# Kernel optimization log

Measured on AMD Instinct MI355X. Metric: run time of the kernel, lower is better.

## Reference

```python
import jax, jax.numpy as jnp
import numpy as np
from math import factorial

N_NODES = 20000
N_EDGES = 80000
NUM_GRAPHS = 64
NUM_NEIGHBORS = 3.8
POOL_NODES = 4.0  # num_nodes=4 constant in source forward

# ---------------- real Wigner 3j (e3nn-style, Frobenius norm 1) ----------------

def _w3j_complex(j1, j2, j3, m1, m2, m3):
    if m1 + m2 + m3 != 0:
        return 0.0
    t1 = j2 - m1 - j3; t2 = j1 + m2 - j3; t3 = j1 + j2 - j3
    t4 = j1 - m1; t5 = j2 + m2
    tmin = max(0, t1, t2); tmax = min(t3, t4, t5)
    if tmin > tmax:
        return 0.0
    s = 0.0
    for t in range(tmin, tmax + 1):
        s += (-1.0) ** t / (factorial(t) * factorial(t - t1) * factorial(t - t2)
                            * factorial(t3 - t) * factorial(t4 - t) * factorial(t5 - t))
    tri = (factorial(j1 + j2 - j3) * factorial(j1 - j2 + j3) * factorial(-j1 + j2 + j3)
           / factorial(j1 + j2 + j3 + 1))
    norm = np.sqrt(tri * factorial(j1 + m1) * factorial(j1 - m1) * factorial(j2 + m2)
                   * factorial(j2 - m2) * factorial(j3 + m3) * factorial(j3 - m3))
    return (-1.0) ** (j1 - j2 - m3) * norm * s


def _real_basis(l):
    U = np.zeros((2 * l + 1, 2 * l + 1), dtype=np.complex128)
    U[l, l] = 1.0
    for m in range(1, l + 1):
        U[l + m, l + m] = (-1) ** m / np.sqrt(2.0)
        U[l + m, l - m] = 1.0 / np.sqrt(2.0)
        U[l - m, l - m] = 1j / np.sqrt(2.0)
        U[l - m, l + m] = -1j * (-1) ** m / np.sqrt(2.0)
    return U

_W3J_CACHE = {}

def w3j(l1, l2, l3):
    key = (l1, l2, l3)
    if key not in _W3J_CACHE:
        C = np.zeros((2 * l1 + 1, 2 * l2 + 1, 2 * l3 + 1), dtype=np.complex128)
        for m1 in range(-l1, l1 + 1):
            for m2 in range(-l2, l2 + 1):
                m3 = -(m1 + m2)
                if -l3 <= m3 <= l3:
                    C[m1 + l1, m2 + l2, m3 + l3] = _w3j_complex(l1, l2, l3, m1, m2, m3)
        C = np.einsum('ia,jb,kc,abc->ijk', _real_basis(l1), _real_basis(l2), _real_basis(l3), C)
        C = np.real((-1j) ** (l1 + l2 + l3) * C)
        _W3J_CACHE[key] = jnp.asarray(C, dtype=jnp.float32)
    return _W3J_CACHE[key]

# ---------------- irreps bookkeeping ----------------
SH        = [(1, 0, 1), (1, 1, -1), (1, 2, 1), (1, 3, -1)]            # 1x0e+1x1o+1x2e+1x3o (dim 16)
GATE1_IN  = [(16,0,1),(16,0,-1),(8,0,1),(8,0,-1),(8,0,1),(8,0,-1),(16,1,-1),(16,1,1)]  # dim 160
GATE1_OUT = [(16,0,1),(16,0,1),(16,1,-1),(16,1,1)]                     # dim 128
GATE2_IN  = [(16,0,1),(16,0,-1),(6,0,1),(6,0,-1),(6,0,1),(6,0,-1),(12,1,-1),(12,1,1)]  # dim 128
GATE2_OUT = [(16,0,1),(16,0,1),(12,1,-1),(12,1,1)]                     # dim 104
OUT_FINAL = [(1, 0, 1)]


def slices(irreps):
    out = []; o = 0
    for m, l, p in irreps:
        d = m * (2 * l + 1); out.append((o, o + d)); o += d
    return out


def tp_paths(ir1, ir2, iro):
    paths = []
    for i1, (m1, l1, p1) in enumerate(ir1):
        for i2, (m2, l2, p2) in enumerate(ir2):
            for io, (mo, lo, po) in enumerate(iro):
                if po == p1 * p2 and abs(l1 - l2) <= lo <= l1 + l2:
                    paths.append((i1, i2, io))
    fan = [0] * len(iro)
    for i1, i2, io in paths:
        fan[io] += ir1[i1][0] * ir2[i2][0]
    numel = sum(ir1[i1][0] * ir2[i2][0] * iro[io][0] for i1, i2, io in paths)
    return paths, fan, numel


def tensor_product(x1, x2, weights, ir1, ir2, iro):
    # FullyConnectedTensorProduct, component norm, element path normalization
    paths, fan, numel = tp_paths(ir1, ir2, iro)
    s1, s2 = slices(ir1), slices(ir2)
    E = x1.shape[0]
    out_parts = [jnp.zeros((E, m * (2 * l + 1)), x1.dtype) for m, l, p in iro]
    wofs = 0
    for i1, i2, io in paths:
        m1, l1, _ = ir1[i1]; m2, l2, _ = ir2[i2]; mo, lo, _ = iro[io]
        n = m1 * m2 * mo
        w = weights[:, wofs:wofs + n].reshape(E, m1, m2, mo); wofs += n
        a = x1[:, s1[i1][0]:s1[i1][1]].reshape(E, m1, 2 * l1 + 1)
        b = x2[:, s2[i2][0]:s2[i2][1]].reshape(E, m2, 2 * l2 + 1)
        C = w3j(l1, l2, lo)
        pw = np.sqrt((2 * lo + 1) / fan[io])
        seg = jnp.einsum('eui,evj,ijk,euvw->ewk', a, b, C, w) * pw
        out_parts[io] = out_parts[io] + seg.reshape(E, mo * (2 * lo + 1))
    return jnp.concatenate(out_parts, axis=1)

# ---------------- activations / gate ----------------
_xs = np.linspace(-8.0, 8.0, 100001)
_pdf = np.exp(-0.5 * _xs ** 2) / np.sqrt(2 * np.pi)
TANH_NORM = float(1.0 / np.sqrt(np.sum(np.tanh(_xs) ** 2 * _pdf) * (_xs[1] - _xs[0])))
SQRT2 = float(np.sqrt(2.0))
ACT = {'relu': lambda t: jnp.maximum(t, 0.0) * SQRT2,
       'abs':  lambda t: jnp.abs(t),
       'tanh': lambda t: jnp.tanh(t) * TANH_NORM}


def gate_fn(x, scalars, gates, gated):
    o = 0; outs = []
    for m, a in scalars:
        outs.append(ACT[a](x[:, o:o + m])); o += m
    gv = []
    for m, a in gates:
        gv.append(ACT[a](x[:, o:o + m])); o += m
    g = jnp.concatenate(gv, axis=-1)
    gi = 0
    for m, l in gated:
        d = 2 * l + 1
        feat = x[:, o:o + m * d].reshape(-1, m, d)
        outs.append((feat * g[:, gi:gi + m, None]).reshape(-1, m * d))
        o += m * d; gi += m
    return jnp.concatenate(outs, axis=-1)

# ---------------- edge features ----------------

def sh_component(v):
    # real spherical harmonics l=0..3, 'component' normalization, unit input
    x, y, z = v[:, 0], v[:, 1], v[:, 2]
    s3, s5, s15 = np.sqrt(3.0), np.sqrt(5.0), np.sqrt(15.0)
    s7, s42, s70, s105 = np.sqrt(7.0), np.sqrt(42.0), np.sqrt(70.0), np.sqrt(105.0)
    Y0 = jnp.ones_like(x)[:, None]
    Y1 = jnp.stack([s3 * y, s3 * z, s3 * x], -1)
    Y2 = jnp.stack([s15 * x * y, s15 * y * z, 0.5 * s5 * (3 * z * z - 1.0),
                    s15 * x * z, 0.5 * s15 * (x * x - y * y)], -1)
    Y3 = jnp.stack([0.25 * s70 * y * (3 * x * x - y * y), s105 * x * y * z,
                    0.25 * s42 * y * (5 * z * z - 1.0), 0.5 * s7 * z * (5 * z * z - 3.0),
                    0.25 * s42 * x * (5 * z * z - 1.0), 0.5 * s105 * z * (x * x - y * y),
                    0.25 * s70 * x * (x * x - 3 * y * y)], -1)
    return jnp.concatenate([Y0, Y1, Y2, Y3], -1)  # [E,16]


def soft_one_hot(r):
    # soft_one_hot_linspace(start=0.5,end=2.5,number=3,basis='smooth_finite',cutoff=True)
    values = np.linspace(0.5, 2.5, 5)[1:-1]
    step = values[1] - values[0]
    diff = (r[:, None] - values) / step
    def f(u):
        return jnp.where(u > 0, jnp.exp(-1.0 / jnp.where(u > 0, u, 1.0)), 0.0)
    y = 1.14136 * np.exp(2.0) * f(diff + 1.0) * f(1.0 - diff)
    return y * np.sqrt(3.0)


def fc(x, w1, w2):
    # e3nn FullyConnectedNet([3,256,numel], relu)
    h = jnp.maximum(x @ (w1 / np.sqrt(w1.shape[0])), 0.0) * SQRT2
    return h @ (w2 / np.sqrt(w2.shape[0]))


def convolution(node_feats, edge_src, edge_dst, edge_attr, edge_scalars, w1, w2, ir_in, ir_out, n_nodes):
    weight = fc(edge_scalars, w1, w2)                                   # [E, numel]
    ef = tensor_product(node_feats[edge_src], edge_attr, weight, ir_in, SH, ir_out)
    return jax.ops.segment_sum(ef, edge_dst, num_segments=n_nodes) / np.sqrt(NUM_NEIGHBORS)


def _forward(pos, w1_1, w2_1, w1_2, w2_2, w1_3, w2_3, edge_src, edge_dst, batch):
    N = pos.shape[0]
    vec = pos[edge_src] - pos[edge_dst]
    r = jnp.sqrt(jnp.sum(vec * vec, axis=1) + 1e-12)
    unit = vec / r[:, None]
    edge_attr = sh_component(unit)
    edge_scalars = soft_one_hot(r)
    x = jax.ops.segment_sum(edge_attr, edge_dst, num_segments=N) / np.sqrt(NUM_NEIGHBORS)
    x = convolution(x, edge_src, edge_dst, edge_attr, edge_scalars, w1_1, w2_1, SH, GATE1_IN, N)
    x = gate_fn(x, [(16, 'relu'), (16, 'abs')], [(8, 'relu'), (8, 'tanh'), (8, 'relu'), (8, 'tanh')], [(16, 1), (16, 1)])
    x = convolution(x, edge_src, edge_dst, edge_attr, edge_scalars, w1_2, w2_2, GATE1_OUT, GATE2_IN, N)
    x = gate_fn(x, [(16, 'relu'), (16, 'abs')], [(6, 'relu'), (6, 'tanh'), (6, 'relu'), (6, 'tanh')], [(12, 1), (12, 1)])
    x = convolution(x, edge_src, edge_dst, edge_attr, edge_scalars, w1_3, w2_3, GATE2_OUT, OUT_FINAL, N)
    x = jax.ops.segment_sum(x, batch, num_segments=NUM_GRAPHS) / np.sqrt(POOL_NODES)
    return jax.nn.sigmoid(x)


def setup_inputs():
    key = jax.random.key(0)
    ks = jax.random.split(key, 10)
    pos = jax.random.normal(ks[0], (N_NODES, 3), jnp.float32) * 1.5
    edge_src = jax.random.randint(ks[1], (N_EDGES,), 0, N_NODES)
    edge_dst = jax.random.randint(ks[2], (N_EDGES,), 0, N_NODES)
    batch = jnp.sort(jax.random.randint(ks[3], (N_NODES,), 0, NUM_GRAPHS))
    _, _, n1 = tp_paths(SH, SH, GATE1_IN)
    _, _, n2 = tp_paths(GATE1_OUT, SH, GATE2_IN)
    _, _, n3 = tp_paths(GATE2_OUT, SH, OUT_FINAL)
    w1_1 = jax.random.normal(ks[4], (3, 256), jnp.float32)
    w2_1 = jax.random.normal(ks[5], (256, n1), jnp.float32)
    w1_2 = jax.random.normal(ks[6], (3, 256), jnp.float32)
    w2_2 = jax.random.normal(ks[7], (256, n2), jnp.float32)
    w1_3 = jax.random.normal(ks[8], (3, 256), jnp.float32)
    w2_3 = jax.random.normal(ks[9], (256, n3), jnp.float32)
    return {'pos': pos, 'w1_1': w1_1, 'w2_1': w2_1, 'w1_2': w1_2, 'w2_2': w2_2,
            'w1_3': w1_3, 'w2_3': w2_3, 'edge_src': edge_src, 'edge_dst': edge_dst, 'batch': batch}


def reference(pos, w1_1, w2_1, w1_2, w2_2, w1_3, w2_3, edge_src, edge_dst, batch):
    return _forward(pos, w1_1, w2_1, w1_2, w2_2, w1_3, w2_3, edge_src, edge_dst, batch)
```

## Files before the change

### kernel.cpp

```cpp
#include <hip/hip_runtime.h>
#include <math.h>

#define NNODE 20000
#define NEDGE 80000
#define NGRAPH 64

#define OFF_TANH  656
#define OFF_CNT   660
#define OFF_GSUM  664
#define OFF_HIST  7680
#define OFF_OFFS  9728
#define OFF_CUR   11784
#define OFF_EATTR 14336
#define OFF_RBUF  1294336
#define OFF_EINFO 1374336
#define OFF_X0    1694336
#define OFF_Y1    2014336
#define OFF_Y2    5214336
#define OFF_X1    7774336
#define OFF_X2    10334336
#define OFF_TAB   12414336

#define T000 0
#define T110 1
#define T220 10
#define T330 35
#define T011 84
#define T101 93
#define T111 102
#define T121 129
#define T211 174
#define T231 219
#define T321 324
#define T221 429
#define T331 504

#define INV_SQRT_NEIGH 0.5129891760425771f
#define SQRT2F 1.4142135623730951f

struct TabD { int l1,l2,l3,off; };
constexpr TabD HTABS[13] = {
  {0,0,0,T000},{1,1,0,T110},{2,2,0,T220},{3,3,0,T330},
  {0,1,1,T011},{1,0,1,T101},{1,1,1,T111},{1,2,1,T121},
  {2,1,1,T211},{2,3,1,T231},{3,2,1,T321},{2,2,1,T221},{3,3,1,T331}
};

struct CoreD { short a_off, b_off; short l1,l2,l3; short tab; short coff; short m1; };
struct PathD { short core; short wofs, wend, ooff; short mo, lo; float pw; };

constexpr CoreD HCORES1[13] = {
  {0,0, 0,0,0, T000, 0, 1},
  {0,1, 0,1,1, T011, 1, 1},
  {1,0, 1,0,1, T101, 4, 1},
  {1,1, 1,1,0, T110, 7, 1},
  {1,1, 1,1,1, T111, 8, 1},
  {1,4, 1,2,1, T121, 11, 1},
  {4,1, 2,1,1, T211, 14, 1},
  {4,4, 2,2,0, T220, 17, 1},
  {4,4, 2,2,1, T221, 18, 1},
  {4,9, 2,3,1, T231, 21, 1},
  {9,4, 3,2,1, T321, 24, 1},
  {9,9, 3,3,0, T330, 27, 1},
  {9,9, 3,3,1, T331, 28, 1}
};
#define PWR 0.7071067811865476f
constexpr PathD HPATHS1[21] = {
  {0,  0, 16,  0,16,0,0.5f},
  {0, 16, 24, 32, 8,0,0.5f},
  {0, 24, 32, 48, 8,0,0.5f},
  {1, 32, 48, 64,16,1,PWR},
  {2, 48, 64, 64,16,1,PWR},
  {3, 64, 80,  0,16,0,0.5f},
  {3, 80, 88, 32, 8,0,0.5f},
  {3, 88, 96, 48, 8,0,0.5f},
  {4, 96,112,112,16,1,1.0f},
  {5,112,128, 64,16,1,PWR},
  {6,128,144, 64,16,1,PWR},
  {7,144,160,  0,16,0,0.5f},
  {7,160,168, 32, 8,0,0.5f},
  {7,168,176, 48, 8,0,0.5f},
  {8,176,192,112,16,1,1.0f},
  {9,192,208, 64,16,1,PWR},
  {10,208,224,64,16,1,PWR},
  {11,224,240, 0,16,0,0.5f},
  {11,240,248,32, 8,0,0.5f},
  {11,248,256,48, 8,0,0.5f},
  {12,256,272,112,16,1,1.0f}
};

constexpr CoreD HCORES2[12] = {
  {0,0,  0,0,0, T000, 0,   16},
  {0,1,  0,1,1, T011, 16,  16},
  {16,0, 0,0,0, T000, 64,  16},
  {16,1, 0,1,1, T011, 80,  16},
  {32,0, 1,0,1, T101, 128, 16},
  {32,1, 1,1,0, T110, 176, 16},
  {32,1, 1,1,1, T111, 192, 16},
  {32,4, 1,2,1, T121, 240, 16},
  {80,0, 1,0,1, T101, 288, 16},
  {80,1, 1,1,0, T110, 336, 16},
  {80,1, 1,1,1, T111, 352, 16},
  {80,4, 1,2,1, T121, 400, 16}
};
#define PA 0.14433756729740643f
#define PB 0.25f
#define PC 0.19364916731037085f
constexpr PathD HPATHS2[20] = {
  {0,   0, 256,  0,16,0,PA},
  {0, 256, 352, 32, 6,0,PA},
  {0, 352, 448, 44, 6,0,PA},
  {1, 448, 640, 56,12,1,PC},
  {2, 640, 896,  0,16,0,PA},
  {2, 896, 992, 32, 6,0,PA},
  {2, 992,1088, 44, 6,0,PA},
  {3,1088,1280, 56,12,1,PC},
  {4,1280,1472, 56,12,1,PC},
  {5,1472,1728,  0,16,0,PA},
  {5,1728,1824, 32, 6,0,PA},
  {5,1824,1920, 44, 6,0,PA},
  {6,1920,2112, 92,12,1,PB},
  {7,2112,2304, 56,12,1,PC},
  {8,2304,2496, 92,12,1,PB},
  {9,2496,2752, 16,16,0,PB},
  {9,2752,2848, 38, 6,0,PB},
  {9,2848,2944, 50, 6,0,PB},
  {10,2944,3136,56,12,1,PC},
  {11,3136,3328,92,12,1,PB}
};

constexpr CoreD HCORES3[3] = {
  {0,0,  0,0,0, T000, 0,  16},
  {16,0, 0,0,0, T000, 16, 16},
  {32,1, 1,1,0, T110, 32, 12}
};
#define PD 0.15075567228888181f
constexpr PathD HPATHS3[3] = {
  {0, 0,16, 0,1,0,PD},
  {1,16,32, 0,1,0,PD},
  {2,32,44, 0,1,0,PD}
};

constexpr double FACT[9] = {1.0,1.0,2.0,6.0,24.0,120.0,720.0,5040.0,40320.0};

constexpr double csqrt_(double x){
  if(x<=0.0) return 0.0;
  double g = (x<1.0)? 1.0 : x;
  for(int i=0;i<40;i++) g = 0.5*(g + x/g);
  return g;
}

constexpr double cw3j_(int j1,int j2,int j3,int m1,int m2,int m3){
  if(m1+m2+m3!=0) return 0.0;
  int t1=j2-m1-j3, t2=j1+m2-j3, t3=j1+j2-j3, t4=j1-m1, t5=j2+m2;
  int tmin=t1>0?t1:0; if(t2>tmin) tmin=t2;
  int tmax=t3<t4?t3:t4; if(t5<tmax) tmax=t5;
  if(tmin>tmax) return 0.0;
  double s=0.0;
  for(int t=tmin;t<=tmax;++t){
    double d=FACT[t]*FACT[t-t1]*FACT[t-t2]*FACT[t3-t]*FACT[t4-t]*FACT[t5-t];
    s += ((t&1)? -1.0:1.0)/d;
  }
  double tri=FACT[j1+j2-j3]*FACT[j1-j2+j3]*FACT[-j1+j2+j3]/FACT[j1+j2+j3+1];
  double nrm=csqrt_(tri*FACT[j1+m1]*FACT[j1-m1]*FACT[j2+m2]*FACT[j2-m2]*FACT[j3+m3]*FACT[j3-m3]);
  return (((j1-j2-m3)&1)? -1.0:1.0)*nrm*s;
}

constexpr int curow_(int l,int i,int* a,double* re,double* im){
  const double is2=0.7071067811865475;
  int m=i-l;
  if(m==0){ a[0]=l; re[0]=1.0; im[0]=0.0; return 1; }
  if(m>0){
    a[0]=l+m; re[0]=((m&1)? -is2:is2); im[0]=0.0;
    a[1]=l-m; re[1]=is2; im[1]=0.0; return 2;
  }
  int mm=-m;
  a[0]=l-mm; re[0]=0.0; im[0]=is2;
  a[1]=l+mm; re[1]=0.0; im[1]=((mm&1)? is2:-is2);
  return 2;
}

constexpr float cw3j_elem_(int l1,int l2,int l3,int i,int j,int k){
  int aa[2]={0,0},bb[2]={0,0},cc[2]={0,0};
  double ar[2]={0,0},ai[2]={0,0},br[2]={0,0},bi[2]={0,0},cr[2]={0,0},ci[2]={0,0};
  int na=curow_(l1,i,aa,ar,ai);
  int nb=curow_(l2,j,bb,br,bi);
  int nc=curow_(l3,k,cc,cr,ci);
  double accr=0.0, acci=0.0;
  for(int x=0;x<na;x++)for(int y=0;y<nb;y++)for(int w=0;w<nc;w++){
    double wv=cw3j_(l1,l2,l3, aa[x]-l1, bb[y]-l2, cc[w]-l3);
    if(wv==0.0) continue;
    double pr=ar[x]*br[y]-ai[x]*bi[y];
    double pi=ar[x]*bi[y]+ai[x]*br[y];
    double qr=pr*cr[w]-pi*ci[w];
    double qi=pr*ci[w]+pi*cr[w];
    accr+=qr*wv; acci+=qi*wv;
  }
  int Lm=(l1+l2+l3)&3;
  double res = (Lm==0)? accr : (Lm==1)? acci : (Lm==2)? -accr : -acci;
  return (float)res;
}

struct WApart { float v[429]; };
constexpr WApart gen_wa_(){
  WApart o{};
  for(int t=0;t<11;t++){
    int l1=HTABS[t].l1,l2=HTABS[t].l2,l3=HTABS[t].l3;
    int n2=2*l2+1,n3=2*l3+1;
    int tot=(2*l1+1)*n2*n3;
    for(int z=0;z<tot;z++){
      int i=z/(n2*n3), j=(z/n3)%n2, k=z%n3;
      o.v[HTABS[t].off+z]=cw3j_elem_(l1,l2,l3,i,j,k);
    }
  }
  return o;
}
struct WBpart { float v[222]; };
constexpr WBpart gen_wb_(){
  WBpart o{};
  for(int t=11;t<13;t++){
    int l1=HTABS[t].l1,l2=HTABS[t].l2,l3=HTABS[t].l3;
    int n2=2*l2+1,n3=2*l3+1;
    int tot=(2*l1+1)*n2*n3;
    for(int z=0;z<tot;z++){
      int i=z/(n2*n3), j=(z/n3)%n2, k=z%n3;
      o.v[HTABS[t].off-429+z]=cw3j_elem_(l1,l2,l3,i,j,k);
    }
  }
  return o;
}
constexpr WApart WAC = gen_wa_();
constexpr WBpart WBC = gen_wb_();
struct W3Full { float v[651]; };
constexpr W3Full gen_wfull_(){
  W3Full f{};
  for(int i=0;i<429;i++) f.v[i]=WAC.v[i];
  for(int i=0;i<222;i++) f.v[429+i]=WBC.v[i];
  return f;
}
__constant__ W3Full W3JC = gen_wfull_();

template<int NW> struct PwArr { float v[NW]; };
template<int NW,int NP>
constexpr PwArr<NW> gen_pw_(const PathD (&P)[NP]){
  PwArr<NW> a{};
  for(int p=0;p<NP;p++)
    for(int j=P[p].wofs;j<P[p].wend;j++) a.v[j]=P[p].pw;
  return a;
}
__constant__ PwArr<272>  PWC1 = gen_pw_<272>(HPATHS1);
__constant__ PwArr<3328> PWC2 = gen_pw_<3328>(HPATHS2);
__constant__ PwArr<44>   PWC3 = gen_pw_<44>(HPATHS3);

struct OutSeg { int mult, l; };
constexpr OutSeg OSEG1[8] = {{16,0},{16,0},{8,0},{8,0},{8,0},{8,0},{16,1},{16,1}};
constexpr OutSeg OSEG2[8] = {{16,0},{16,0},{6,0},{6,0},{6,0},{6,0},{12,1},{12,1}};
constexpr OutSeg OSEG3[1] = {{1,0}};

struct Ent2 { int jb, cb, nu; };
template<int NCOL,int NENT,int NW> struct ColMetaT {
  int cidx[NCOL+1];
  int obase[NCOL];
  int n3c[NCOL];
  Ent2 ent[NENT];
  int newj[NW];
};

template<int NCOL,int NENT,int NW,int NSEG,int NP,int NC>
constexpr ColMetaT<NCOL,NENT,NW> gen_colmeta_(const OutSeg (&S)[NSEG], const PathD (&P)[NP], const CoreD (&C)[NC]){
  ColMetaT<NCOL,NENT,NW> m{};
  int col=0, cnt=0, o=0, nb=0;
  for(int s=0;s<NSEG;s++){
    int n3=2*S[s].l+1;
    for(int wc=0;wc<S[s].mult;wc++){
      m.cidx[col]=cnt;
      int ob=o+wc*n3;
      m.obase[col]=ob;
      m.n3c[col]=n3;
      for(int p=0;p<NP;p++){
        PathD pd=P[p];
        int pn3=2*pd.lo+1;
        if(pn3!=n3) continue;
        int rel=ob-pd.ooff;
        if(rel<0||rel>=pd.mo*pn3) continue;
        int w=rel/pn3;
        CoreD cd=C[pd.core];
        int m1=cd.m1;
        m.ent[cnt]=Ent2{nb,(int)cd.coff,m1};
        for(int u=0;u<m1;u++) m.newj[pd.wofs + w + u*pd.mo]=nb+u;
        nb+=m1;
        cnt++;
      }
      col++;
    }
    o+=S[s].mult*n3;
  }
  m.cidx[col]=cnt;
  return m;
}

__constant__ ColMetaT<96,272,272>  CMETA1 = gen_colmeta_<96,272,272>(OSEG1, HPATHS1, HCORES1);
__constant__ ColMetaT<80,208,3328> CMETA2 = gen_colmeta_<80,208,3328>(OSEG2, HPATHS2, HCORES2);
__constant__ ColMetaT< 1,  3,  44> CMETA3 = gen_colmeta_< 1,  3,  44>(OSEG3, HPATHS3, HCORES3);

struct CItem { short aoff, boff, n1, n2, cofs, jstep, woff, pad; };
struct CArr1 { CItem it[31]; };
constexpr CArr1 gen_c1_(){
  CArr1 a{}; int s=0;
  for(int cn=0;cn<13;cn++){
    CoreD cd=HCORES1[cn];
    int n1=2*cd.l1+1,n2=2*cd.l2+1,n3=2*cd.l3+1;
    for(int k=0;k<n3;k++){
      a.it[s]=CItem{cd.a_off,cd.b_off,(short)n1,(short)n2,(short)(cd.tab+k),(short)n3,(short)(cd.coff+k),0};
      s++;
    }
  }
  return a;
}
__constant__ CArr1 CIT1 = gen_c1_();

struct Fam { short b_off, tab, n1, n2, n3, goff; };
constexpr Fam GF2[6]={
  {0,T000,1,1,1,0},{1,T011,1,3,3,1},{0,T101,3,1,3,4},
  {1,T110,3,3,1,13},{1,T111,3,3,3,16},{4,T121,3,5,3,25}};
constexpr Fam GF3[2]={{0,T000,1,1,1,0},{1,T110,3,3,1,1}};
struct CoreG { short fam,a_off,m1,coff; };
constexpr CoreG CG2[12]={
  {0,0,16,0},{1,0,16,16},{0,16,16,64},{1,16,16,80},
  {2,32,16,128},{3,32,16,176},{4,32,16,192},{5,32,16,240},
  {2,80,16,288},{3,80,16,336},{4,80,16,352},{5,80,16,400}};
constexpr CoreG CG3[3]={{0,0,16,0},{0,16,16,16},{1,32,12,32}};

struct GItem { short boff, cofs, n2, jstep; };
template<int NG> struct GArrT { GItem it[NG]; };
template<int NG,int NF>
constexpr GArrT<NG> gen_g_(const Fam (&F)[NF]){
  GArrT<NG> a{}; int s=0;
  for(int f=0;f<NF;f++){
    for(int i=0;i<F[f].n1;i++)for(int k=0;k<F[f].n3;k++){
      a.it[s]=GItem{F[f].b_off,(short)(F[f].tab + i*F[f].n2*F[f].n3 + k),F[f].n2,F[f].n3};
      s++;
    }
  }
  return a;
}
__constant__ GArrT<34> GIT2=gen_g_<34>(GF2);
__constant__ GArrT<4>  GIT3=gen_g_<4>(GF3);

struct OItem { short aoff, gofs, n1, n3, woff, pad; };
template<int NO> struct OArrT { OItem it[NO]; };
template<int NO,int NC,int NF>
constexpr OArrT<NO> gen_o_(const CoreG (&C)[NC], const Fam (&F)[NF]){
  OArrT<NO> a{}; int s=0;
  for(int cn=0;cn<NC;cn++){
    Fam f=F[C[cn].fam];
    for(int k=0;k<f.n3;k++)for(int u=0;u<C[cn].m1;u++){
      a.it[s]=OItem{(short)(C[cn].a_off+u*f.n1),(short)(f.goff+k),f.n1,f.n3,
                    (short)(C[cn].coff+k*C[cn].m1+u),0};
      s++;
    }
  }
  return a;
}
__constant__ OArrT<448> OIT2=gen_o_<448,12,6>(CG2,GF2);
__constant__ OArrT<44>  OIT3=gen_o_<44,3,2>(CG3,GF3);

template<int CNT,int N3,int NCOLS>
__device__ __forceinline__ void apply1_col(const Ent2* __restrict__ ep, const float* __restrict__ T0,
    const float* __restrict__ crb, float fr, float&a0,float&a1,float&a2){
  const float* tja=T0+ep[0].jb;
  float wv[CNT];
  #pragma unroll
  for(int t=0;t<CNT;t++){
    float w0=tja[t], w1=tja[t+NCOLS];
    wv[t]=w0+fr*(w1-w0);
  }
  #pragma unroll
  for(int t=0;t<CNT;t++){
    const float* cr=crb+ep[t].cb;
    a0=fmaf(wv[t],cr[0],a0);
    if constexpr(N3==3){ a1=fmaf(wv[t],cr[1],a1); a2=fmaf(wv[t],cr[2],a2); }
  }
}
__device__ __forceinline__ void apply1_dyn(const Ent2* __restrict__ ep, int cnt, int n3,
    const float* __restrict__ T0, const float* __restrict__ crb, float fr, int NCOLS,
    float&a0,float&a1,float&a2){
  const float* tja=T0+ep[0].jb;
  for(int t=0;t<cnt;t++){
    float w0=tja[t], w1=tja[t+NCOLS];
    float w=w0+fr*(w1-w0);
    const float* cr=crb+ep[t].cb;
    a0=fmaf(w,cr[0],a0);
    if(n3==3){ a1=fmaf(w,cr[1],a1); a2=fmaf(w,cr[2],a2); }
  }
}
template<int CNT,int N3,int NCOLS>
__device__ __forceinline__ void apply2_col(const Ent2* __restrict__ ep, const float* __restrict__ T0,
    const float* __restrict__ crb, float fr, float&a0,float&a1,float&a2){
  if constexpr(N3==1){
    float s0=0.0f,s1=0.0f,s2=0.0f,s3=0.0f;
    #pragma unroll
    for(int t=0;t<CNT;t++){
      const float* cr=crb+ep[t].cb;
      const float* tj=T0+ep[t].jb;
      #pragma unroll
      for(int uu=0;uu<16;uu+=4){
        float4 w0=*(const float4*)(tj+uu);
        float4 w1=*(const float4*)(tj+NCOLS+uu);
        float4 cv=*(const float4*)(cr+uu);
        float w;
        w=w0.x+fr*(w1.x-w0.x); s0=fmaf(w,cv.x,s0);
        w=w0.y+fr*(w1.y-w0.y); s1=fmaf(w,cv.y,s1);
        w=w0.z+fr*(w1.z-w0.z); s2=fmaf(w,cv.z,s2);
        w=w0.w+fr*(w1.w-w0.w); s3=fmaf(w,cv.w,s3);
      }
    }
    a0=(s0+s1)+(s2+s3);
  } else {
    #pragma unroll
    for(int t=0;t<CNT;t++){
      const float* cr=crb+ep[t].cb;
      const float* tj=T0+ep[t].jb;
      #pragma unroll
      for(int uu=0;uu<16;uu+=4){
        float4 w0=*(const float4*)(tj+uu);
        float4 w1=*(const float4*)(tj+NCOLS+uu);
        float4 c0=*(const float4*)(cr+uu);
        float4 c1=*(const float4*)(cr+16+uu);
        float4 c2=*(const float4*)(cr+32+uu);
        float w;
        w=w0.x+fr*(w1.x-w0.x); a0=fmaf(w,c0.x,a0); a1=fmaf(w,c1.x,a1); a2=fmaf(w,c2.x,a2);
        w=w0.y+fr*(w1.y-w0.y); a0=fmaf(w,c0.y,a0); a1=fmaf(w,c1.y,a1); a2=fmaf(w,c2.y,a2);
        w=w0.z+fr*(w1.z-w0.z); a0=fmaf(w,c0.z,a0); a1=fmaf(w,c1.z,a1); a2=fmaf(w,c2.z,a2);
        w=w0.w+fr*(w1.w-w0.w); a0=fmaf(w,c0.w,a0); a1=fmaf(w,c1.w,a1); a2=fmaf(w,c2.w,a2);
      }
    }
  }
}
__device__ __forceinline__ void apply2_dyn(const Ent2* __restrict__ ep, int cnt, int n3,
    const float* __restrict__ T0, const float* __restrict__ crb, float fr, int NCOLS,
    float&a0,float&a1,float&a2){
  for(int t=0;t<cnt;t++){
    const float* cr=crb+ep[t].cb;
    const float* tj=T0+ep[t].jb;
    #pragma unroll
    for(int uu=0;uu<16;uu+=4){
      float4 w0=*(const float4*)(tj+uu);
      float4 w1=*(const float4*)(tj+NCOLS+uu);
      float w;
      if(n3==1){
        float4 cv=*(const float4*)(cr+uu);
        w=w0.x+fr*(w1.x-w0.x); a0=fmaf(w,cv.x,a0);
        w=w0.y+fr*(w1.y-w0.y); a0=fmaf(w,cv.y,a0);
        w=w0.z+fr*(w1.z-w0.z); a0=fmaf(w,cv.z,a0);
        w=w0.w+fr*(w1.w-w0.w); a0=fmaf(w,cv.w,a0);
      } else {
        float4 c0=*(const float4*)(cr+uu);
        float4 c1=*(const float4*)(cr+16+uu);
        float4 c2=*(const float4*)(cr+32+uu);
        w=w0.x+fr*(w1.x-w0.x); a0=fmaf(w,c0.x,a0); a1=fmaf(w,c1.x,a1); a2=fmaf(w,c2.x,a2);
        w=w0.y+fr*(w1.y-w0.y); a0=fmaf(w,c0.y,a0); a1=fmaf(w,c1.y,a1); a2=fmaf(w,c2.y,a2);
        w=w0.z+fr*(w1.z-w0.z); a0=fmaf(w,c0.z,a0); a1=fmaf(w,c1.z,a1); a2=fmaf(w,c2.z,a2);
        w=w0.w+fr*(w1.w-w0.w); a0=fmaf(w,c0.w,a0); a1=fmaf(w,c1.w,a1); a2=fmaf(w,c2.w,a2);
      }
    }
  }
}

template<int JT>
__device__ __forceinline__ void ldw_(float* w, const float* p){
  if constexpr(JT==2) *(float2*)w = *(const float2*)p;
  else if constexpr(JT==4) *(float4*)w = *(const float4*)p;
  else { *(float4*)w=*(const float4*)p; *(float4*)(w+4)=*(const float4*)(p+4); }
}
template<int JT>
__device__ __forceinline__ void table_gemm(const float* __restrict__ W2, float* __restrict__ tab,
    int NCOLS, float scale, const float* __restrict__ PW, const int* __restrict__ NJ,
    int jb, const float (*__restrict__ sh_h)[8], int r0, int R){
  float acc[8][JT];
  #pragma unroll
  for(int k=0;k<8;k++)
    #pragma unroll
    for(int u=0;u<JT;u++) acc[k][u]=0.0f;
  const float* w2p=W2+jb;
  float w0[JT], w1[JT];
  ldw_<JT>(w0, w2p);
  ldw_<JT>(w1, w2p+NCOLS);
  for(int c=0;c<256;c+=2){
    int cp0=(c+2<256)?(c+2):255;
    int cp1=(c+3<256)?(c+3):255;
    float n0[JT], n1[JT];
    ldw_<JT>(n0, w2p+(size_t)cp0*NCOLS);
    ldw_<JT>(n1, w2p+(size_t)cp1*NCOLS);
    float h0[8], h1[8];
    *(float4*)&h0[0]=*(const float4*)&sh_h[c][0];
    *(float4*)&h0[4]=*(const float4*)&sh_h[c][4];
    *(float4*)&h1[0]=*(const float4*)&sh_h[c+1][0];
    *(float4*)&h1[4]=*(const float4*)&sh_h[c+1][4];
    #pragma unroll
    for(int k=0;k<8;k++)
      #pragma unroll
      for(int u=0;u<JT;u++)
        acc[k][u]=fmaf(h0[k],w0[u],acc[k][u]);
    #pragma unroll
    for(int k=0;k<8;k++)
      #pragma unroll
      for(int u=0;u<JT;u++)
        acc[k][u]=fmaf(h1[k],w1[u],acc[k][u]);
    #pragma unroll
    for(int u=0;u<JT;u++){ w0[u]=n0[u]; w1[u]=n1[u]; }
  }
  #pragma unroll
  for(int u=0;u<JT;u++){
    float cs=scale*PW[jb+u];
    int jn=NJ[jb+u];
    #pragma unroll
    for(int k=0;k<8;k++){
      int ri=r0+k;
      if(ri<R) tab[(size_t)ri*NCOLS+jn]=acc[k][u]*cs;
    }
  }
}

__global__ __launch_bounds__(256) void k_tables(
    const float* __restrict__ W1_1, const float* __restrict__ W2_1, float* __restrict__ T1,
    const float* __restrict__ W1_2, const float* __restrict__ W2_2, float* __restrict__ T2,
    const float* __restrict__ W1_3, const float* __restrict__ W2_3, float* __restrict__ T3,
    int R, int NR, float* __restrict__ ws){
  int tid=threadIdx.x;
  int by=blockIdx.y;
  if(by==9){
    if(blockIdx.x!=0) return;
    for(int i=tid;i<(728-OFF_CNT);i+=256) ws[OFF_CNT+i]=0.0f;
    for(int i=tid;i<(13832-OFF_HIST);i+=256) ws[OFF_HIST+i]=0.0f;
    __shared__ double red[256];
    double loc=0.0;
    for(int i=tid;i<=100000;i+=256){
      float x=-8.0f+16.0f*(float)i/100000.0f;
      float th=tanhf(x);
      float pdf=expf(-0.5f*x*x)*0.3989422804014327f;
      loc += (double)(th*th*pdf);
    }
    red[tid]=loc; __syncthreads();
    for(int s=128;s>0;s>>=1){ if(tid<s) red[tid]+=red[tid+s]; __syncthreads(); }
    if(tid==0) ws[OFF_TANH]=(float)(1.0/sqrt(red[0]*(16.0/100000.0)));
    return;
  }
  int conv, jb0, jlim;
  const float* W1; const float* W2; float* tab; int NCOLS; float scale;
  if(by<7){ conv=2; jb0=by*512; jlim=(jb0+512<3328)?(jb0+512):3328;
            W1=W1_2; W2=W2_2; tab=T2; NCOLS=3328; scale=INV_SQRT_NEIGH; }
  else if(by==7){ conv=1; jb0=0; jlim=272; W1=W1_1; W2=W2_1; tab=T1; NCOLS=272;  scale=INV_SQRT_NEIGH; }
  else { conv=3; jb0=0; jlim=44; W1=W1_3; W2=W2_3; tab=T3; NCOLS=44;   scale=INV_SQRT_NEIGH*0.5f; }

  __shared__ float sh_h[256][8];
  int r0=blockIdx.x*8;
  {
    int c=tid;
    float wa=W1[c], wb=W1[256+c], wc=W1[512+c];
    const float A=(float)(1.14136*7.38905609893065*1.7320508075688772);
    #pragma unroll
    for(int k=0;k<8;k++){
      int ri=r0+k;
      float r=0.5f+2.0f*(float)ri/(float)NR;
      float sv[3];
      #pragma unroll
      for(int j=0;j<3;j++){
        float v=1.0f+0.5f*(float)j;
        float diff=(r-v)*2.0f;
        float u1=diff+1.0f, u2=1.0f-diff;
        float f1=(u1>0.0f)? expf(-1.0f/u1):0.0f;
        float f2=(u2>0.0f)? expf(-1.0f/u2):0.0f;
        sv[j]=A*f1*f2;
      }
      float hv=sv[0]*wa+sv[1]*wb+sv[2]*wc;
      hv=fmaxf(hv*0.5773502691896258f,0.0f)*(SQRT2F*0.0625f);
      sh_h[c][k]=hv;
    }
  }
  __syncthreads();
  const float* PW=(conv==1)? PWC1.v : (conv==2)? PWC2.v : PWC3.v;
  const int* NJ=(conv==1)? CMETA1.newj : (conv==2)? CMETA2.newj : CMETA3.newj;
  int jb=jb0+tid*2;
  if(jb+2<=jlim)
    table_gemm<2>(W2,tab,NCOLS,scale,PW,NJ,jb,sh_h,r0,R);
}

__global__ void k_edge(const float* __restrict__ pos, const int* __restrict__ esrc,
                       const int* __restrict__ edst, float* __restrict__ ws, int NR){
  int e = blockIdx.x*256 + threadIdx.x;
  if(e>=NEDGE) return;
  float* eattr=ws+OFF_EATTR;
  float* x0=ws+OFF_X0;
  int s=esrc[e], d=edst[e];
  float x=pos[3*s]-pos[3*d], y=pos[3*s+1]-pos[3*d+1], z=pos[3*s+2]-pos[3*d+2];
  float r=sqrtf(x*x+y*y+z*z+1e-12f);
  float iv=1.0f/r; x*=iv; y*=iv; z*=iv;
  const float s3=1.7320508075688772f, s5=2.2360679774997896f, s15=3.872983346207417f;
  const float s7=2.6457513110645907f, s42=6.48074069840786f, s70=8.366600265340756f, s105=10.246950765959598f;
  float Y[16];
  Y[0]=1.0f;
  Y[1]=s3*y; Y[2]=s3*z; Y[3]=s3*x;
  Y[4]=s15*x*y; Y[5]=s15*y*z; Y[6]=0.5f*s5*(3.0f*z*z-1.0f); Y[7]=s15*x*z; Y[8]=0.5f*s15*(x*x-y*y);
  Y[9]=0.25f*s70*y*(3.0f*x*x-y*y); Y[10]=s105*x*y*z; Y[11]=0.25f*s42*y*(5.0f*z*z-1.0f);
  Y[12]=0.5f*s7*z*(5.0f*z*z-3.0f); Y[13]=0.25f*s42*x*(5.0f*z*z-1.0f);
  Y[14]=0.5f*s105*z*(x*x-y*y); Y[15]=0.25f*s70*x*(x*x-3.0f*y*y);
  float4* ep=(float4*)(eattr+(size_t)e*16);
  ep[0]=make_float4(Y[0],Y[1],Y[2],Y[3]);
  ep[1]=make_float4(Y[4],Y[5],Y[6],Y[7]);
  ep[2]=make_float4(Y[8],Y[9],Y[10],Y[11]);
  ep[3]=make_float4(Y[12],Y[13],Y[14],Y[15]);
  #pragma unroll
  for(int i=0;i<16;i++)
    atomicAdd(&x0[(size_t)d*16+i], Y[i]*INV_SQRT_NEIGH);
  ws[OFF_RBUF+e]=r;
  if(r>0.5f && r<2.5f){
    float t=(r-0.5f)*((float)NR*0.5f);
    int i0=min((int)t, NR-1);
    atomicAdd((int*)(ws+OFF_HIST)+i0, 1);
  }
}

__global__ void k_scan(float* __restrict__ ws, int NR){
  __shared__ int sd[2048];
  int t=threadIdx.x;
  int* hist=(int*)(ws+OFF_HIST);
  int* offs=(int*)(ws+OFF_OFFS);
  int i1=t, i2=t+1024;
  sd[i1]=(i1<NR)? hist[i1]:0;
  sd[i2]=(i2<NR)? hist[i2]:0;
  __syncthreads();
  for(int d=1; d<2048; d<<=1){
    int v1=(i1>=d)? sd[i1-d]:0;
    int v2=(i2>=d)? sd[i2-d]:0;
    __syncthreads();
    sd[i1]+=v1; sd[i2]+=v2;
    __syncthreads();
  }
  if(i1<NR) offs[i1]=(i1==0)?0:sd[i1-1];
  if(i2<NR) offs[i2]=sd[i2-1];
  if(t==0){ offs[NR]=sd[NR-1]; *((int*)(ws+OFF_CNT))=sd[NR-1]; }
}

__global__ void k_scatter(const int* __restrict__ esrc, const int* __restrict__ edst,
                          float* __restrict__ ws, int NR){
  int e=blockIdx.x*256+threadIdx.x;
  if(e>=NEDGE) return;
  float r=ws[OFF_RBUF+e];
  if(!(r>0.5f && r<2.5f)) return;
  float t=(r-0.5f)*((float)NR*0.5f);
  int i0=min((int)t, NR-1);
  int* offs=(int*)(ws+OFF_OFFS);
  int* cur=(int*)(ws+OFF_CUR);
  int p=offs[i0]+atomicAdd(&cur[i0],1);
  int4 v; v.x=esrc[e]; v.y=edst[e]; v.z=e; v.w=__float_as_int(t);
  ((int4*)(ws+OFF_EINFO))[p]=v;
}

template<int CONV,int DY,int D_IN,int D_OUT,int CSTRIDE,int NCOL,int NCOLS,bool FINAL>
__global__ __launch_bounds__(256,4) void k_conv(
    const float* __restrict__ xin, const float* __restrict__ TAB,
    float* __restrict__ yout, const int* __restrict__ batchp,
    float* __restrict__ ws, int NR)
{
  constexpr int APAD = D_IN+4;
  constexpr int NGP  = (CONV==2)?36:4;
  constexpr int YST  = (CONV==3)?132:4;
  constexpr int NGV  = (CONV==2)?32:((CONV==3)?24:1);
  __shared__ float sh_a[8][APAD];
  __shared__ float sh_b[8][20];
  __shared__ float sh_core[8][CSTRIDE];
  __shared__ float sh_g[8][NGP];
  __shared__ float sh_gv[8][NGV];
  __shared__ float sh_y[8][YST];
  __shared__ float sh_red[8];
  __shared__ int sh_src[8], sh_dst[8], sh_eid[8];
  __shared__ float sh_t[8];

  int tid=threadIdx.x;
  int nact=*(const int*)(ws+OFF_CNT);
  int base=blockIdx.x*8;
  if(base>=nact) return;
  int ne=min(8, nact-base);

  if(tid<8){
    int src=0,dst=0,eid=-1; float tv=0.0f;
    if(tid<ne){
      int4 v=((const int4*)(ws+OFF_EINFO))[base+tid];
      src=v.x; dst=v.y; eid=v.z; tv=__int_as_float(v.w);
    }
    sh_src[tid]=src; sh_dst[tid]=dst; sh_eid[tid]=eid; sh_t[tid]=tv;
    if constexpr(CONV==3) sh_red[tid]=0.0f;
  }
  __syncthreads();

  if(tid<32){
    int idx=tid>>2, c4=tid&3;
    int eid=sh_eid[idx];
    float4 v=make_float4(0.f,0.f,0.f,0.f);
    if(eid>=0) v=((const float4*)(ws+OFF_EATTR+(size_t)eid*16))[c4];
    *(float4*)&sh_b[idx][c4*4]=v;
  }
  if constexpr(CONV==1){
    if(tid>=32 && tid<64){
      int t2=tid-32; int idx=t2>>2, c4=t2&3;
      float4 v=make_float4(0.f,0.f,0.f,0.f);
      if(sh_eid[idx]>=0) v=((const float4*)(xin+(size_t)sh_src[idx]*16))[c4];
      *(float4*)&sh_a[idx][c4*4]=v;
    }
  } else {
    constexpr int YQ=DY/4;
    for(int z=tid; z<8*YQ; z+=256){
      int idx=z/YQ, c4=z-idx*YQ;
      float4 v=make_float4(0.f,0.f,0.f,0.f);
      if(sh_eid[idx]>=0) v=((const float4*)(xin+(size_t)sh_src[idx]*DY))[c4];
      if constexpr(CONV==2) *(float4*)&sh_core[idx][c4*4]=v;
      else                  *(float4*)&sh_y[idx][c4*4]=v;
    }
  }
  __syncthreads();

  if constexpr(CONV==1){
    constexpr int NIT=31;
    for(int z=tid; z<8*NIT; z+=256){
      int idx=z/NIT, rem=z-idx*NIT;
      CItem it=CIT1.it[rem];
      float acc=0.0f;
      for(int i=0;i<it.n1;i++){
        float av=sh_a[idx][it.aoff+i];
        int cb=it.cofs + i*it.n2*it.jstep;
        for(int j=0;j<it.n2;j++)
          acc += av*sh_b[idx][it.boff+j]*W3JC.v[cb + j*it.jstep];
      }
      sh_core[idx][it.woff]=acc;
    }
    __syncthreads();
  } else {
    float TN=ws[OFF_TANH];
    for(int z=tid; z<8*NGV; z+=256){
      int idx=z/NGV, m=z-idx*NGV;
      const float* yr=(CONV==2)? &sh_core[idx][0] : &sh_y[idx][0];
      float u=yr[32+m];
      bool th=(CONV==2)? (((m>>3)&1)!=0) : (((m/6)&1)!=0);
      sh_gv[idx][m]= th? tanhf(u)*TN : fmaxf(u,0.0f)*SQRT2F;
    }
    constexpr int NG=(CONV==2)?34:4;
    for(int z=tid; z<8*NG; z+=256){
      int idx=z/NG, rem=z-idx*NG;
      GItem it=(CONV==2)? GIT2.it[rem] : GIT3.it[rem];
      float acc=0.0f;
      for(int j=0;j<it.n2;j++)
        acc += sh_b[idx][it.boff+j]*W3JC.v[it.cofs + j*it.jstep];
      sh_g[idx][rem]=acc;
    }
    __syncthreads();
    for(int z=tid; z<8*D_IN; z+=256){
      int idx=z/D_IN, o=z-idx*D_IN;
      const float* yr=(CONV==2)? &sh_core[idx][0] : &sh_y[idx][0];
      float val;
      if(o<16) val=fmaxf(yr[o],0.0f)*SQRT2F;
      else if(o<32) val=fabsf(yr[o]);
      else {
        if constexpr(CONV==2){
          int gi=(o<80)? (o-32)/3 : 16+(o-80)/3;
          val=yr[o+32]*sh_gv[idx][gi];
        } else {
          int gi=(o<68)? (o-32)/3 : 12+(o-68)/3;
          val=yr[o+24]*sh_gv[idx][gi];
        }
      }
      sh_a[idx][o]=val;
    }
    __syncthreads();
    constexpr int NO=(CONV==2)?448:44;
    for(int z=tid; z<8*NO; z+=256){
      int idx=z/NO, rem=z-idx*NO;
      OItem it=(CONV==2)? OIT2.it[rem] : OIT3.it[rem];
      float acc=0.0f;
      #pragma unroll 3
      for(int i=0;i<it.n1;i++)
        acc += sh_a[idx][it.aoff+i]*sh_g[idx][it.gofs + i*it.n3];
      sh_core[idx][it.woff]=acc;
    }
    __syncthreads();
  }

  if constexpr(CONV==3){
    if(tid<88){
      int e3=tid&7, c=tid>>3;
      float tv=sh_t[e3];
      int i0=min((int)tv, NR-1);
      float fr=tv-(float)i0;
      const float* tj=TAB+(size_t)i0*NCOLS + c*4;
      float4 w0=*(const float4*)tj;
      float4 w1=*(const float4*)(tj+NCOLS);
      float4 cv=*(const float4*)(&sh_core[e3][c*4]);
      float p;
      p  = (w0.x+fr*(w1.x-w0.x))*cv.x;
      p += (w0.y+fr*(w1.y-w0.y))*cv.y;
      p += (w0.z+fr*(w1.z-w0.z))*cv.z;
      p += (w0.w+fr*(w1.w-w0.w))*cv.w;
      atomicAdd(&sh_red[e3], p);
    }
    __syncthreads();
    if(tid<ne) atomicAdd(&ws[OFF_GSUM+batchp[sh_dst[tid]]], sh_red[tid]);
  } else {
    int e=tid&7;
    float tv=sh_t[e];
    int i0=min((int)tv, NR-1);
    float fr=tv-(float)i0;
    const float* T0=TAB+(size_t)i0*NCOLS;
    const float* crb=&sh_core[e][0];
    int dstv=sh_dst[e];
    bool act=(e<ne);

    for(int q=tid; q<8*NCOL; q+=256){
      int c=q>>3;
      int s0,s1,ob,n3;
      const Ent2* entp;
      if constexpr(CONV==1){ s0=CMETA1.cidx[c]; s1=CMETA1.cidx[c+1]; ob=CMETA1.obase[c]; n3=CMETA1.n3c[c]; entp=CMETA1.ent; }
      else                 { s0=CMETA2.cidx[c]; s1=CMETA2.cidx[c+1]; ob=CMETA2.obase[c]; n3=CMETA2.n3c[c]; entp=CMETA2.ent; }
      int cnt=s1-s0;
      if(!cnt) continue;
      float a0=0.0f,a1=0.0f,a2=0.0f;
      const Ent2* ep=entp+s0;
      if constexpr(CONV==1){
        if(n3==1){
          switch(cnt){
            case 4: apply1_col<4,1,272>(ep,T0,crb,fr,a0,a1,a2); break;
            default: apply1_dyn(ep,cnt,1,T0,crb,fr,272,a0,a1,a2); break;
          }
        } else {
          switch(cnt){
            case 6: apply1_col<6,3,272>(ep,T0,crb,fr,a0,a1,a2); break;
            case 3: apply1_col<3,3,272>(ep,T0,crb,fr,a0,a1,a2); break;
            default: apply1_dyn(ep,cnt,3,T0,crb,fr,272,a0,a1,a2); break;
          }
        }
      } else {
        if(n3==1){
          switch(cnt){
            case 3: apply2_col<3,1,3328>(ep,T0,crb,fr,a0,a1,a2); break;
            case 1: apply2_col<1,1,3328>(ep,T0,crb,fr,a0,a1,a2); break;
            default: apply2_dyn(ep,cnt,1,T0,crb,fr,3328,a0,a1,a2); break;
          }
        } else {
          switch(cnt){
            case 5: apply2_col<5,3,3328>(ep,T0,crb,fr,a0,a1,a2); break;
            case 3: apply2_col<3,3,3328>(ep,T0,crb,fr,a0,a1,a2); break;
            default: apply2_dyn(ep,cnt,3,T0,crb,fr,3328,a0,a1,a2); break;
          }
        }
      }
      if(act){
        float* yp=&yout[(size_t)dstv*D_OUT+ob];
        atomicAdd(yp, a0);
        if(n3==3){ atomicAdd(yp+1, a1); atomicAdd(yp+2, a2); }
      }
    }
  }
}

__global__ void k_sig(const float* __restrict__ ws, float* __restrict__ out){
  int g=threadIdx.x;
  if(g<NGRAPH){
    float v=ws[OFF_GSUM+g];
    out[g]=1.0f/(1.0f+expf(-v));
  }
}

extern "C" void kernel_launch(void* const* d_in, const int* in_sizes, int n_in,
                              void* d_out, int out_size, void* d_ws, size_t ws_size,
                              hipStream_t stream){
  const float* pos =(const float*)d_in[0];
  const float* w1_1=(const float*)d_in[1];
  const float* w2_1=(const float*)d_in[2];
  const float* w1_2=(const float*)d_in[3];
  const float* w2_2=(const float*)d_in[4];
  const float* w1_3=(const float*)d_in[5];
  const float* w2_3=(const float*)d_in[6];
  const int* esrc=(const int*)d_in[7];
  const int* edst=(const int*)d_in[8];
  const int* batch=(const int*)d_in[9];
  float* ws=(float*)d_ws;
  float* out=(float*)d_out;

  long availRows = ((long)(ws_size/4) - (long)OFF_TAB)/3644L;
  int R = (availRows < 1025L)? (int)availRows : 1025;
  if(R < 9) R = 9;
  int NR = R-1;
  float* TAB1 = ws + OFF_TAB;
  float* TAB2 = TAB1 + (size_t)R*272;
  float* TAB3 = TAB2 + (size_t)R*3328;

  hipMemsetAsync(ws+OFF_X0, 0, (size_t)(OFF_X1-OFF_X0)*sizeof(float), stream);

  k_tables<<<dim3((R+7)/8,10),256,0,stream>>>(
      w1_1,w2_1,TAB1, w1_2,w2_2,TAB2, w1_3,w2_3,TAB3, R,NR, ws);
  k_edge<<<(NEDGE+255)/256,256,0,stream>>>(pos, esrc, edst, ws, NR);
  k_scan<<<1,1024,0,stream>>>(ws, NR);
  k_scatter<<<(NEDGE+255)/256,256,0,stream>>>(esrc, edst, ws, NR);

  k_conv<1, 16, 16,160, 33, 96, 272,false><<<(NEDGE+7)/8,256,0,stream>>>(
      ws+OFF_X0, TAB1, ws+OFF_Y1, batch, ws, NR);

  k_conv<2,160,128,128,452, 80,3328,false><<<(NEDGE+7)/8,256,0,stream>>>(
      ws+OFF_Y1, TAB2, ws+OFF_Y2, batch, ws, NR);

  k_conv<3,128,104,  1, 68,  1, 44,true ><<<(NEDGE+7)/8,256,0,stream>>>(
      ws+OFF_Y2, TAB3, nullptr, batch, ws, NR);

  k_sig<<<1,64,0,stream>>>(ws, out);
}
```

Before: 396.3 us.

## Merge table, edge and zeroing work into one front kernel launch

Combines the table-building kernel, the per-edge spherical-harmonics and histogram kernel, and the zeroing of the Y1/Y2 buffers into a single launch with a 1D block-index dispatch. The large memset is split so only X0 is cleared by memset, while Y1/Y2 are zeroed by extra blocks running alongside the other work. The counter and histogram clearing moves out of the kernel into small memsets. The N3==1 accumulation in apply2_col now uses a single serial accumulator instead of four partial sums, which lengthens the FMA dependency chain and slightly changes summation order. The goal is to cut launch overhead and let independent stages share the GPU at the same time.

```diff
diff --git a/kernel.cpp b/kernel.cpp
--- a/kernel.cpp
+++ b/kernel.cpp
@@ -396,38 +396,25 @@
 template<int CNT,int N3,int NCOLS>
 __device__ __forceinline__ void apply2_col(const Ent2* __restrict__ ep, const float* __restrict__ T0,
     const float* __restrict__ crb, float fr, float&a0,float&a1,float&a2){
-  if constexpr(N3==1){
-    float s0=0.0f,s1=0.0f,s2=0.0f,s3=0.0f;
+  #pragma unroll
+  for(int t=0;t<CNT;t++){
+    const float* cr=crb+ep[t].cb;
+    const float* tj=T0+ep[t].jb;
     #pragma unroll
-    for(int t=0;t<CNT;t++){
-      const float* cr=crb+ep[t].cb;
-      const float* tj=T0+ep[t].jb;
-      #pragma unroll
-      for(int uu=0;uu<16;uu+=4){
-        float4 w0=*(const float4*)(tj+uu);
-        float4 w1=*(const float4*)(tj+NCOLS+uu);
+    for(int uu=0;uu<16;uu+=4){
+      float4 w0=*(const float4*)(tj+uu);
+      float4 w1=*(const float4*)(tj+NCOLS+uu);
+      float w;
+      if constexpr(N3==1){
         float4 cv=*(const float4*)(cr+uu);
-        float w;
-        w=w0.x+fr*(w1.x-w0.x); s0=fmaf(w,cv.x,s0);
-        w=w0.y+fr*(w1.y-w0.y); s1=fmaf(w,cv.y,s1);
-        w=w0.z+fr*(w1.z-w0.z); s2=fmaf(w,cv.z,s2);
-        w=w0.w+fr*(w1.w-w0.w); s3=fmaf(w,cv.w,s3);
-      }
-    }
-    a0=(s0+s1)+(s2+s3);
-  } else {
-    #pragma unroll
-    for(int t=0;t<CNT;t++){
-      const float* cr=crb+ep[t].cb;
-      const float* tj=T0+ep[t].jb;
-      #pragma unroll
-      for(int uu=0;uu<16;uu+=4){
-        float4 w0=*(const float4*)(tj+uu);
-        float4 w1=*(const float4*)(tj+NCOLS+uu);
+        w=w0.x+fr*(w1.x-w0.x); a0=fmaf(w,cv.x,a0);
+        w=w0.y+fr*(w1.y-w0.y); a0=fmaf(w,cv.y,a0);
+        w=w0.z+fr*(w1.z-w0.z); a0=fmaf(w,cv.z,a0);
+        w=w0.w+fr*(w1.w-w0.w); a0=fmaf(w,cv.w,a0);
+      } else {
         float4 c0=*(const float4*)(cr+uu);
         float4 c1=*(const float4*)(cr+16+uu);
         float4 c2=*(const float4*)(cr+32+uu);
-        float w;
         w=w0.x+fr*(w1.x-w0.x); a0=fmaf(w,c0.x,a0); a1=fmaf(w,c1.x,a1); a2=fmaf(w,c2.x,a2);
         w=w0.y+fr*(w1.y-w0.y); a0=fmaf(w,c0.y,a0); a1=fmaf(w,c1.y,a1); a2=fmaf(w,c2.y,a2);
         w=w0.z+fr*(w1.z-w0.z); a0=fmaf(w,c0.z,a0); a1=fmaf(w,c1.z,a1); a2=fmaf(w,c2.z,a2);
@@ -521,17 +508,64 @@
   }
 }
 
-__global__ __launch_bounds__(256) void k_tables(
+__global__ __launch_bounds__(256) void k_front(
     const float* __restrict__ W1_1, const float* __restrict__ W2_1, float* __restrict__ T1,
     const float* __restrict__ W1_2, const float* __restrict__ W2_2, float* __restrict__ T2,
     const float* __restrict__ W1_3, const float* __restrict__ W2_3, float* __restrict__ T3,
-    int R, int NR, float* __restrict__ ws){
+    const float* __restrict__ pos, const int* __restrict__ esrc, const int* __restrict__ edst,
+    int R, int NR, int NXT, float* __restrict__ ws){
+  __shared__ float sh_h[256][8];
+  int bid=blockIdx.x;
   int tid=threadIdx.x;
-  int by=blockIdx.y;
-  if(by==9){
-    if(blockIdx.x!=0) return;
-    for(int i=tid;i<(728-OFF_CNT);i+=256) ws[OFF_CNT+i]=0.0f;
-    for(int i=tid;i<(13832-OFF_HIST);i+=256) ws[OFF_HIST+i]=0.0f;
+  int NT2=7*NXT;
+
+  if(bid<NT2+2*NXT){
+    int jb0, jlim, xt;
+    const float* W1; const float* W2; float* tab; int NCOLS; float scale;
+    const float* PW; const int* NJ;
+    if(bid<NT2){
+      int s=bid/NXT; xt=bid-s*NXT; jb0=s*512; jlim=(jb0+512<3328)?(jb0+512):3328;
+      W1=W1_2; W2=W2_2; tab=T2; NCOLS=3328; scale=INV_SQRT_NEIGH; PW=PWC2.v; NJ=CMETA2.newj;
+    } else if(bid<NT2+NXT){
+      xt=bid-NT2; jb0=0; jlim=272;
+      W1=W1_1; W2=W2_1; tab=T1; NCOLS=272; scale=INV_SQRT_NEIGH; PW=PWC1.v; NJ=CMETA1.newj;
+    } else {
+      xt=bid-NT2-NXT; jb0=0; jlim=44;
+      W1=W1_3; W2=W2_3; tab=T3; NCOLS=44; scale=INV_SQRT_NEIGH*0.5f; PW=PWC3.v; NJ=CMETA3.newj;
+    }
+    int r0=xt*8;
+    {
+      int c=tid;
+      float wa=W1[c], wb=W1[256+c], wc=W1[512+c];
+      const float A=(float)(1.14136*7.38905609893065*1.7320508075688772);
+      #pragma unroll
+      for(int k=0;k<8;k++){
+        int ri=r0+k;
+        float r=0.5f+2.0f*(float)ri/(float)NR;
+        float sv[3];
+        #pragma unroll
+        for(int j=0;j<3;j++){
+          float v=1.0f+0.5f*(float)j;
+          float diff=(r-v)*2.0f;
+          float u1=diff+1.0f, u2=1.0f-diff;
+          float f1=(u1>0.0f)? expf(-1.0f/u1):0.0f;
+          float f2=(u2>0.0f)? expf(-1.0f/u2):0.0f;
+          sv[j]=A*f1*f2;
+        }
+        float hv=sv[0]*wa+sv[1]*wb+sv[2]*wc;
+        hv=fmaxf(hv*0.5773502691896258f,0.0f)*(SQRT2F*0.0625f);
+        sh_h[c][k]=hv;
+      }
+    }
+    __syncthreads();
+    int jb=jb0+tid*2;
+    if(jb+2<=jlim)
+      table_gemm<2>(W2,tab,NCOLS,scale,PW,NJ,jb,sh_h,r0,R);
+    return;
+  }
+  bid-=NT2+2*NXT;
+
+  if(bid==0){
     __shared__ double red[256];
     double loc=0.0;
     for(int i=tid;i<=100000;i+=256){
@@ -545,78 +579,50 @@
     if(tid==0) ws[OFF_TANH]=(float)(1.0/sqrt(red[0]*(16.0/100000.0)));
     return;
   }
-  int conv, jb0, jlim;
-  const float* W1; const float* W2; float* tab; int NCOLS; float scale;
-  if(by<7){ conv=2; jb0=by*512; jlim=(jb0+512<3328)?(jb0+512):3328;
-            W1=W1_2; W2=W2_2; tab=T2; NCOLS=3328; scale=INV_SQRT_NEIGH; }
-  else if(by==7){ conv=1; jb0=0; jlim=272; W1=W1_1; W2=W2_1; tab=T1; NCOLS=272;  scale=INV_SQRT_NEIGH; }
-  else { conv=3; jb0=0; jlim=44; W1=W1_3; W2=W2_3; tab=T3; NCOLS=44;   scale=INV_SQRT_NEIGH*0.5f; }
-
-  __shared__ float sh_h[256][8];
-  int r0=blockIdx.x*8;
+  bid-=1;
+
+  if(bid<313){
+    int e=bid*256+tid;
+    if(e>=NEDGE) return;
+    float* eattr=ws+OFF_EATTR;
+    float* x0=ws+OFF_X0;
+    int s=esrc[e], d=edst[e];
+    float x=pos[3*s]-pos[3*d], y=pos[3*s+1]-pos[3*d+1], z=pos[3*s+2]-pos[3*d+2];
+    float r=sqrtf(x*x+y*y+z*z+1e-12f);
+    float iv=1.0f/r; x*=iv; y*=iv; z*=iv;
+    const float s3=1.7320508075688772f, s5=2.2360679774997896f, s15=3.872983346207417f;
+    const float s7=2.6457513110645907f, s42=6.48074069840786f, s70=8.366600265340756f, s105=10.246950765959598f;
+    float Y[16];
+    Y[0]=1.0f;
+    Y[1]=s3*y; Y[2]=s3*z; Y[3]=s3*x;
+    Y[4]=s15*x*y; Y[5]=s15*y*z; Y[6]=0.5f*s5*(3.0f*z*z-1.0f); Y[7]=s15*x*z; Y[8]=0.5f*s15*(x*x-y*y);
+    Y[9]=0.25f*s70*y*(3.0f*x*x-y*y); Y[10]=s105*x*y*z; Y[11]=0.25f*s42*y*(5.0f*z*z-1.0f);
+    Y[12]=0.5f*s7*z*(5.0f*z*z-3.0f); Y[13]=0.25f*s42*x*(5.0f*z*z-1.0f);
+    Y[14]=0.5f*s105*z*(x*x-y*y); Y[15]=0.25f*s70*x*(x*x-3.0f*y*y);
+    float4* ep=(float4*)(eattr+(size_t)e*16);
+    ep[0]=make_float4(Y[0],Y[1],Y[2],Y[3]);
+    ep[1]=make_float4(Y[4],Y[5],Y[6],Y[7]);
+    ep[2]=make_float4(Y[8],Y[9],Y[10],Y[11]);
+    ep[3]=make_float4(Y[12],Y[13],Y[14],Y[15]);
+    #pragma unroll
+    for(int i=0;i<16;i++)
+      atomicAdd(&x0[(size_t)d*16+i], Y[i]*INV_SQRT_NEIGH);
+    ws[OFF_RBUF+e]=r;
+    if(r>0.5f && r<2.5f){
+      float t=(r-0.5f)*((float)NR*0.5f);
+      int i0=min((int)t, NR-1);
+      atomicAdd((int*)(ws+OFF_HIST)+i0, 1);
+    }
+    return;
+  }
+  bid-=313;
+
   {
-    int c=tid;
-    float wa=W1[c], wb=W1[256+c], wc=W1[512+c];
-    const float A=(float)(1.14136*7.38905609893065*1.7320508075688772);
-    #pragma unroll
-    for(int k=0;k<8;k++){
-      int ri=r0+k;
-      float r=0.5f+2.0f*(float)ri/(float)NR;
-      float sv[3];
-      #pragma unroll
-      for(int j=0;j<3;j++){
-        float v=1.0f+0.5f*(float)j;
-        float diff=(r-v)*2.0f;
-        float u1=diff+1.0f, u2=1.0f-diff;
-        float f1=(u1>0.0f)? expf(-1.0f/u1):0.0f;
-        float f2=(u2>0.0f)? expf(-1.0f/u2):0.0f;
-        sv[j]=A*f1*f2;
-      }
-      float hv=sv[0]*wa+sv[1]*wb+sv[2]*wc;
-      hv=fmaxf(hv*0.5773502691896258f,0.0f)*(SQRT2F*0.0625f);
-      sh_h[c][k]=hv;
-    }
-  }
-  __syncthreads();
-  const float* PW=(conv==1)? PWC1.v : (conv==2)? PWC2.v : PWC3.v;
-  const int* NJ=(conv==1)? CMETA1.newj : (conv==2)? CMETA2.newj : CMETA3.newj;
-  int jb=jb0+tid*2;
-  if(jb+2<=jlim)
-    table_gemm<2>(W2,tab,NCOLS,scale,PW,NJ,jb,sh_h,r0,R);
-}
-
-__global__ void k_edge(const float* __restrict__ pos, const int* __restrict__ esrc,
-                       const int* __restrict__ edst, float* __restrict__ ws, int NR){
-  int e = blockIdx.x*256 + threadIdx.x;
-  if(e>=NEDGE) return;
-  float* eattr=ws+OFF_EATTR;
-  float* x0=ws+OFF_X0;
-  int s=esrc[e], d=edst[e];
-  float x=pos[3*s]-pos[3*d], y=pos[3*s+1]-pos[3*d+1], z=pos[3*s+2]-pos[3*d+2];
-  float r=sqrtf(x*x+y*y+z*z+1e-12f);
-  float iv=1.0f/r; x*=iv; y*=iv; z*=iv;
-  const float s3=1.7320508075688772f, s5=2.2360679774997896f, s15=3.872983346207417f;
-  const float s7=2.6457513110645907f, s42=6.48074069840786f, s70=8.366600265340756f, s105=10.246950765959598f;
-  float Y[16];
-  Y[0]=1.0f;
-  Y[1]=s3*y; Y[2]=s3*z; Y[3]=s3*x;
-  Y[4]=s15*x*y; Y[5]=s15*y*z; Y[6]=0.5f*s5*(3.0f*z*z-1.0f); Y[7]=s15*x*z; Y[8]=0.5f*s15*(x*x-y*y);
-  Y[9]=0.25f*s70*y*(3.0f*x*x-y*y); Y[10]=s105*x*y*z; Y[11]=0.25f*s42*y*(5.0f*z*z-1.0f);
-  Y[12]=0.5f*s7*z*(5.0f*z*z-3.0f); Y[13]=0.25f*s42*x*(5.0f*z*z-1.0f);
-  Y[14]=0.5f*s105*z*(x*x-y*y); Y[15]=0.25f*s70*x*(x*x-3.0f*y*y);
-  float4* ep=(float4*)(eattr+(size_t)e*16);
-  ep[0]=make_float4(Y[0],Y[1],Y[2],Y[3]);
-  ep[1]=make_float4(Y[4],Y[5],Y[6],Y[7]);
-  ep[2]=make_float4(Y[8],Y[9],Y[10],Y[11]);
-  ep[3]=make_float4(Y[12],Y[13],Y[14],Y[15]);
-  #pragma unroll
-  for(int i=0;i<16;i++)
-    atomicAdd(&x0[(size_t)d*16+i], Y[i]*INV_SQRT_NEIGH);
-  ws[OFF_RBUF+e]=r;
-  if(r>0.5f && r<2.5f){
-    float t=(r-0.5f)*((float)NR*0.5f);
-    int i0=min((int)t, NR-1);
-    atomicAdd((int*)(ws+OFF_HIST)+i0, 1);
+    float4* dst=(float4*)(ws+OFF_Y1);
+    size_t n4=(size_t)(OFF_X1-OFF_Y1)/4;
+    float4 z4=make_float4(0.f,0.f,0.f,0.f);
+    for(size_t i=(size_t)bid*256+tid; i<n4; i+=(size_t)256*256)
+      dst[i]=z4;
   }
 }
 
@@ -888,15 +894,19 @@
   int R = (availRows < 1025L)? (int)availRows : 1025;
   if(R < 9) R = 9;
   int NR = R-1;
+  int NXT = (R+7)/8;
   float* TAB1 = ws + OFF_TAB;
   float* TAB2 = TAB1 + (size_t)R*272;
   float* TAB3 = TAB2 + (size_t)R*3328;
 
-  hipMemsetAsync(ws+OFF_X0, 0, (size_t)(OFF_X1-OFF_X0)*sizeof(float), stream);
-
-  k_tables<<<dim3((R+7)/8,10),256,0,stream>>>(
-      w1_1,w2_1,TAB1, w1_2,w2_2,TAB2, w1_3,w2_3,TAB3, R,NR, ws);
-  k_edge<<<(NEDGE+255)/256,256,0,stream>>>(pos, esrc, edst, ws, NR);
+  hipMemsetAsync(ws+OFF_CNT, 0, (size_t)(728-OFF_CNT)*sizeof(float), stream);
+  hipMemsetAsync(ws+OFF_HIST, 0, (size_t)(13832-OFF_HIST)*sizeof(float), stream);
+  hipMemsetAsync(ws+OFF_X0, 0, (size_t)(OFF_Y1-OFF_X0)*sizeof(float), stream);
+
+  int nblk = 9*NXT + 1 + 313 + 256;
+  k_front<<<nblk,256,0,stream>>>(
+      w1_1,w2_1,TAB1, w1_2,w2_2,TAB2, w1_3,w2_3,TAB3,
+      pos, esrc, edst, R, NR, NXT, ws);
   k_scan<<<1,1024,0,stream>>>(ws, NR);
   k_scatter<<<(NEDGE+255)/256,256,0,stream>>>(esrc, edst, ws, NR);
 
```

New measurement: 338.1 us, median of 3. -14.7%, faster.
